# Kernel optimization log

Hardware: AMD Instinct MI355X
Metric: run time of the kernel (lower is better)

Reference implementation:

```python
import jax, jax.numpy as jnp
import numpy as np

B, S, D, H = 2, 2048, 768, 12
HD = D // H


def setup_inputs() -> dict:
    key = jax.random.key(0)
    ks = jax.random.split(key, 8)
    scale = 1.0 / np.sqrt(D)
    inp = {
        "q": jax.random.normal(ks[0], (B, S, D), jnp.float32),
        "k": jax.random.normal(ks[1], (B, S, D), jnp.float32),
        "v": jax.random.normal(ks[2], (B, S, D), jnp.float32),
        # causal mask: 1.0 where attention is disallowed (upper triangle)
        "mask": jnp.triu(jnp.ones((S, S), jnp.float32), k=1)[None, None, :, :],
        "Wq": jax.random.normal(ks[3], (D, D), jnp.float32) * scale,
        "bq": jnp.zeros((D,), jnp.float32),
        "Wk": jax.random.normal(ks[4], (D, D), jnp.float32) * scale,
        "bk": jnp.zeros((D,), jnp.float32),
        "Wv": jax.random.normal(ks[5], (D, D), jnp.float32) * scale,
        "bv": jnp.zeros((D,), jnp.float32),
        "Wo": jax.random.normal(ks[6], (D, D), jnp.float32) * scale,
        "bo": jnp.zeros((D,), jnp.float32),
    }
    return inp


def _split_heads(x):
    # [B, S, D] -> [B, H, S, HD]
    b, s, _ = x.shape
    return x.reshape(b, s, H, HD).transpose(0, 2, 1, 3)


def reference(q, k, v, mask, Wq, bq, Wk, bk, Wv, bv, Wo, bo):
    qh = _split_heads(q @ Wq + bq)
    kh = _split_heads(k @ Wk + bk)
    vh = _split_heads(v @ Wv + bv)
    scale = 1.0 / jnp.sqrt(jnp.asarray(HD, qh.dtype))
    # [B, H, Sq, Sk] — full attention matrix, as in the original
    scores = jnp.einsum("bhqd,bhkd->bhqk", qh, kh) * scale
    scores = scores + mask * -1e9
    attn = jax.nn.softmax(scores, axis=-1)  # dropout is identity at inference
    out = jnp.einsum("bhqk,bhkd->bhqd", attn, vh)
    out = out.transpose(0, 2, 1, 3).reshape(q.shape[0], -1, D)
    return out @ Wo + bo
```

## Files before the change

### kernel.cpp

```cpp
#include <hip/hip_runtime.h>

#define SEQ    2048
#define NB     2
#define DMODEL 768
#define NH     12
#define HDIM   64
#define BS     (NB * SEQ)

typedef __bf16  bf16x8  __attribute__((ext_vector_type(8)));
typedef ushort  ushort8 __attribute__((ext_vector_type(8)));
typedef float   floatx4 __attribute__((ext_vector_type(4)));

#define GLOBAL_AS __attribute__((address_space(1)))
#define LDS_AS    __attribute__((address_space(3)))

union PackU8 { ushort u[8]; uint4 v; };
union PackU4 { ushort u[4]; uint2 v; };

__device__ __forceinline__ ushort f2bf(float x) {
    union { float f; unsigned u; } t; t.f = x;
    unsigned r = t.u + 0x7fffu + ((t.u >> 16) & 1u);
    return (ushort)(r >> 16);
}

__device__ __forceinline__ bf16x8 ld_frag(const ushort* p) {
    return __builtin_bit_cast(bf16x8, *(const ushort8*)p);
}

__global__ void convert_x(const float* __restrict__ q, const float* __restrict__ k,
                          const float* __restrict__ v,
                          ushort* __restrict__ qo, ushort* __restrict__ ko,
                          ushort* __restrict__ vo)
{
    const float* src = blockIdx.z == 0 ? q : blockIdx.z == 1 ? k : v;
    ushort*      dst = blockIdx.z == 0 ? qo : blockIdx.z == 1 ? ko : vo;
    const int i = (blockIdx.x * 256 + threadIdx.x) * 4;
    const float4 f = *(const float4*)(src + i);
    ushort4 o;
    o.x = f2bf(f.x); o.y = f2bf(f.y); o.z = f2bf(f.z); o.w = f2bf(f.w);
    *(ushort4*)(dst + i) = o;
}

__global__ __launch_bounds__(256)
void convert_wT(const float* __restrict__ wq, const float* __restrict__ wk,
                const float* __restrict__ wv, const float* __restrict__ wo,
                ushort* __restrict__ wtcat, ushort* __restrict__ wto)
{
    __shared__ float Tf[64][69];
    const int z = blockIdx.z;
    const float* w = z == 0 ? wq : z == 1 ? wk : z == 2 ? wv : wo;
    ushort*      o = z < 3 ? wtcat + (size_t)z * DMODEL * DMODEL : wto;
    const int k0 = blockIdx.x * 64, n0 = blockIdx.y * 64;
    const int tid = threadIdx.x;
#pragma unroll
    for (int p = 0; p < 4; ++p) {
        const int idx = tid + p * 256;
        const int r = idx >> 4, c = (idx & 15) * 4;
        const float4 f = *(const float4*)&w[(size_t)(k0 + r) * DMODEL + n0 + c];
        Tf[r][c] = f.x; Tf[r][c + 1] = f.y; Tf[r][c + 2] = f.z; Tf[r][c + 3] = f.w;
    }
    __syncthreads();
#pragma unroll
    for (int p = 0; p < 2; ++p) {
        const int idx = tid + p * 256;
        const int n = idx >> 3, kk = (idx & 7) * 8;
        PackU8 pk;
#pragma unroll
        for (int j = 0; j < 8; ++j) pk.u[j] = f2bf(Tf[kk + j][n]);
        *(uint4*)&o[(size_t)(n0 + n) * DMODEL + k0 + kk] = pk.v;
    }
}

__global__ __launch_bounds__(256)
void gemm_qkv(const ushort* __restrict__ xq, const ushort* __restrict__ xk,
              const ushort* __restrict__ xv, const ushort* __restrict__ WT,
              const float* __restrict__ bq, const float* __restrict__ bk,
              const float* __restrict__ bv,
              ushort* __restrict__ oq, ushort* __restrict__ ok,
              ushort* __restrict__ ov)
{
    __shared__ __align__(16) ushort As[128 * 32];
    __shared__ __align__(16) ushort Bs[128 * 32];

    const int z = blockIdx.y / 6;
    const ushort* X = z == 0 ? xq : z == 1 ? xk : xv;

    const int tid  = threadIdx.x;
    const int lane = tid & 63;
    const int w    = tid >> 6;
    const int l15  = lane & 15;
    const int quad = lane >> 4;
    const int wm   = (w >> 1) * 64;
    const int wn   = (w & 1) * 64;
    const int row0 = blockIdx.x * 128;
    const int col0 = blockIdx.y * 128;

    floatx4 acc[4][4];
    const floatx4 fzero = {0.f, 0.f, 0.f, 0.f};
#pragma unroll
    for (int i = 0; i < 4; ++i)
#pragma unroll
        for (int j = 0; j < 4; ++j) acc[i][j] = fzero;

    const int rin = lane >> 2;
    const int gc  = (lane & 3) * 8;

    for (int k0 = 0; k0 < DMODEL; k0 += 32) {
#pragma unroll
        for (int p = 0; p < 2; ++p) {
            const int ch = w * 2 + p;
            const int r  = ch * 16 + rin;
            __builtin_amdgcn_global_load_lds(
                (const GLOBAL_AS uint*)&X[(size_t)(row0 + r) * DMODEL + k0 + gc],
                (LDS_AS uint*)&As[ch * 512], 16, 0, 0);
            __builtin_amdgcn_global_load_lds(
                (const GLOBAL_AS uint*)&WT[(size_t)(col0 + r) * DMODEL + k0 + gc],
                (LDS_AS uint*)&Bs[ch * 512], 16, 0, 0);
        }
        __syncthreads();

        bf16x8 af[4], bfr[4];
#pragma unroll
        for (int t = 0; t < 4; ++t) {
            af[t]  = ld_frag(&As[(wm + t * 16 + l15) * 32 + quad * 8]);
            bfr[t] = ld_frag(&Bs[(wn + t * 16 + l15) * 32 + quad * 8]);
        }
#pragma unroll
        for (int ti = 0; ti < 4; ++ti)
#pragma unroll
            for (int tj = 0; tj < 4; ++tj)
                acc[ti][tj] = __builtin_amdgcn_mfma_f32_16x16x32_bf16(
                    af[ti], bfr[tj], acc[ti][tj], 0, 0, 0);
        __syncthreads();
    }

    const int c0 = (blockIdx.y % 6) * 128;
    const float*  bias = z == 0 ? bq : z == 1 ? bk : bv;
    ushort*       out  = z == 0 ? oq : z == 1 ? ok : ov;
    const float   sc   = (z == 0) ? 0.18033688f : 1.f;
#pragma unroll
    for (int tj = 0; tj < 4; ++tj) {
        const int c_l = c0 + wn + tj * 16 + l15;
        const float bb = bias[c_l];
        const int h  = c_l >> 6;
        const int dd = c_l & 63;
#pragma unroll
        for (int ti = 0; ti < 4; ++ti) {
#pragma unroll
            for (int ri = 0; ri < 4; ++ri) {
                const int r_g = row0 + wm + ti * 16 + quad * 4 + ri;
                const int b   = r_g >> 11;
                const int s   = r_g & (SEQ - 1);
                out[(((size_t)(b * NH + h) * SEQ + s) << 6) + dd] =
                    f2bf((acc[ti][tj][ri] + bb) * sc);
            }
        }
    }
}

__global__ __launch_bounds__(256)
void gemm_out(const ushort* __restrict__ X, const ushort* __restrict__ WT,
              const float* __restrict__ bias, float* __restrict__ fo)
{
    __shared__ __align__(16) ushort As[64][40];
    __shared__ __align__(16) ushort Bs[128][40];

    const int tid  = threadIdx.x;
    const int lane = tid & 63;
    const int wv   = tid >> 6;
    const int wm   = (wv >> 1) * 32;
    const int wn   = (wv & 1) * 64;
    const int l15  = lane & 15;
    const int quad = lane >> 4;
    const int row0 = blockIdx.x * 64;
    const int col0 = blockIdx.y * 128;

    floatx4 acc[2][4];
    const floatx4 fzero = {0.f, 0.f, 0.f, 0.f};
#pragma unroll
    for (int i = 0; i < 2; ++i)
#pragma unroll
        for (int j = 0; j < 4; ++j) acc[i][j] = fzero;

    const int sr = tid >> 2;
    const int sc = (tid & 3) * 8;

    for (int k0 = 0; k0 < DMODEL; k0 += 32) {
        *(uint4*)&As[sr][sc] = *(const uint4*)&X[(size_t)(row0 + sr) * DMODEL + k0 + sc];
#pragma unroll
        for (int p = 0; p < 2; ++p) {
            const int r = sr + p * 64;
            *(uint4*)&Bs[r][sc] = *(const uint4*)&WT[(size_t)(col0 + r) * DMODEL + k0 + sc];
        }
        __syncthreads();

        bf16x8 af[2], bfr[4];
#pragma unroll
        for (int t = 0; t < 2; ++t)
            af[t] = ld_frag(&As[wm + t * 16 + l15][quad * 8]);
#pragma unroll
        for (int t = 0; t < 4; ++t)
            bfr[t] = ld_frag(&Bs[wn + t * 16 + l15][quad * 8]);
#pragma unroll
        for (int ti = 0; ti < 2; ++ti)
#pragma unroll
            for (int tj = 0; tj < 4; ++tj)
                acc[ti][tj] = __builtin_amdgcn_mfma_f32_16x16x32_bf16(
                    af[ti], bfr[tj], acc[ti][tj], 0, 0, 0);
        __syncthreads();
    }

#pragma unroll
    for (int tj = 0; tj < 4; ++tj) {
        const int c_g = col0 + wn + tj * 16 + l15;
        const float bb = bias[c_g];
#pragma unroll
        for (int ti = 0; ti < 2; ++ti)
#pragma unroll
            for (int ri = 0; ri < 4; ++ri) {
                const int r_g = row0 + wm + ti * 16 + quad * 4 + ri;
                fo[(size_t)r_g * DMODEL + c_g] = acc[ti][tj][ri] + bb;
            }
    }
}

__global__ void transpose_v(const ushort* __restrict__ vh, ushort* __restrict__ vt)
{
    __shared__ __align__(16) ushort T[64][72];
    const int bh = blockIdx.y;
    const int s0 = blockIdx.x * 64;
    const ushort* src = vh + (size_t)bh * SEQ * HDIM;
    ushort*       dst = vt + (size_t)bh * HDIM * SEQ;

#pragma unroll
    for (int p = 0; p < 2; ++p) {
        const int idx = threadIdx.x + p * 256;
        const int r = idx >> 3, c = (idx & 7) * 8;
        *(uint4*)&T[r][c] = *(const uint4*)&src[(size_t)(s0 + r) * HDIM + c];
    }
    __syncthreads();
#pragma unroll
    for (int p = 0; p < 2; ++p) {
        const int idx = threadIdx.x + p * 256;
        const int d = idx >> 3, c = (idx & 7) * 8;
        PackU8 pk;
#pragma unroll
        for (int j = 0; j < 8; ++j) pk.u[j] = T[c + j][d];
        *(uint4*)&dst[(size_t)d * SEQ + s0 + c] = pk.v;
    }
}

__global__ __launch_bounds__(64)
void attn_mfma(const ushort* __restrict__ qh, const ushort* __restrict__ kh,
               const ushort* __restrict__ vt, ushort* __restrict__ ctx)
{
    __shared__ __align__(16) ushort Ks[2][64][64];
    __shared__ __align__(16) ushort Vs[2][64][64];
    __shared__ __align__(16) ushort Ps[32][64];

    const int lane = threadIdx.x;
    const int l15  = lane & 15;
    const int quad = lane >> 4;
    const int e3   = l15 & 7;

    const int id  = blockIdx.x;
    const int xcd = id & 7;
    const int jj  = id >> 3;
    const int g   = jj >> 5;
    const int x   = jj & 31;
    const int bh  = xcd + 8 * g;
    const int b   = bh / NH, h = bh - b * NH;
    const int qA  = x, qB = 63 - x;
    const int nkA = (qA >> 1) + 1;
    const size_t base = (size_t)bh * SEQ * HDIM;

    bf16x8 qA0[2], qA1[2], qB0[2], qB1[2];
#pragma unroll
    for (int ks = 0; ks < 2; ++ks) {
        qA0[ks] = ld_frag(&qh[base + (size_t)(qA * 32 +      l15) * HDIM + ks * 32 + quad * 8]);
        qA1[ks] = ld_frag(&qh[base + (size_t)(qA * 32 + 16 + l15) * HDIM + ks * 32 + quad * 8]);
        qB0[ks] = ld_frag(&qh[base + (size_t)(qB * 32 +      l15) * HDIM + ks * 32 + quad * 8]);
        qB1[ks] = ld_frag(&qh[base + (size_t)(qB * 32 + 16 + l15) * HDIM + ks * 32 + quad * 8]);
    }

    const int sr8  = lane >> 3;
    const int kcol = ((lane & 7) ^ sr8) * 8;

    auto stage = [&](int bufi, int c0s) {
#pragma unroll
        for (int p = 0; p < 8; ++p) {
            __builtin_amdgcn_global_load_lds(
                (const GLOBAL_AS uint*)&kh[base + (size_t)(c0s + 8 * p + sr8) * HDIM + kcol],
                (LDS_AS uint*)&Ks[bufi][8 * p][0], 16, 0, 0);
            __builtin_amdgcn_global_load_lds(
                (const GLOBAL_AS uint*)&vt[base + (size_t)(8 * p + sr8) * SEQ + c0s + kcol],
                (LDS_AS uint*)&Vs[bufi][8 * p][0], 16, 0, 0);
        }
    };

    stage(0, 0);

    float l0 = 0.f, l1 = 0.f;
    floatx4 O[4][2];
    const floatx4 fzero = {0.f, 0.f, 0.f, 0.f};
#pragma unroll
    for (int dj = 0; dj < 4; ++dj) { O[dj][0] = fzero; O[dj][1] = fzero; }

    auto epilogue = [&](int qt) {
        const float i0 = 1.f / l0, i1 = 1.f / l1;
        float ib0[4], ib1[4];
#pragma unroll
        for (int ri = 0; ri < 4; ++ri) {
            ib0[ri] = __shfl(i0, quad * 4 + ri);
            ib1[ri] = __shfl(i1, quad * 4 + ri);
        }
#pragma unroll
        for (int dj = 0; dj < 4; ++dj)
#pragma unroll
            for (int ri = 0; ri < 4; ++ri) {
                const int r0 = qt * 32 + quad * 4 + ri;
                ctx[((size_t)b * SEQ + r0) * DMODEL + h * HDIM + dj * 16 + l15] =
                    f2bf(O[dj][0][ri] * ib0[ri]);
                ctx[((size_t)b * SEQ + r0 + 16) * DMODEL + h * HDIM + dj * 16 + l15] =
                    f2bf(O[dj][1][ri] * ib1[ri]);
            }
    };

    asm volatile("s_waitcnt vmcnt(0)" ::: "memory");

    for (int t = 0; t <= 32; ++t) {
        const int  cur  = t & 1;
        const bool isA  = (t < nkA);
        const int  kt   = isA ? t : t - nkA;
        const int  c0   = kt * 64;
        const bool diag = (t == nkA - 1) || (t == 32);
        const int  qt   = isA ? qA : qB;

        bf16x8 kf[4][2], vf[4][2];
#pragma unroll
        for (int nj = 0; nj < 4; ++nj)
#pragma unroll
            for (int ks = 0; ks < 2; ++ks) {
                kf[nj][ks] = ld_frag(&Ks[cur][nj * 16 + l15][(ks * 32 + quad * 8) ^ (e3 << 3)]);
                vf[nj][ks] = ld_frag(&Vs[cur][nj * 16 + l15][(ks * 32 + quad * 8) ^ (e3 << 3)]);
            }

        if (t < 32) {
            const int kn = (t + 1 < nkA) ? (t + 1) : (t + 1 - nkA);
            stage(cur ^ 1, kn * 64);
        }

        const bf16x8 q0k0 = isA ? qA0[0] : qB0[0];
        const bf16x8 q0k1 = isA ? qA0[1] : qB0[1];
        const bf16x8 q1k0 = isA ? qA1[0] : qB1[0];
        const bf16x8 q1k1 = isA ? qA1[1] : qB1[1];

        floatx4 S[4][2];
        __builtin_amdgcn_s_setprio(1);
#pragma unroll
        for (int nj = 0; nj < 4; ++nj) {
            S[nj][0] = __builtin_amdgcn_mfma_f32_16x16x32_bf16(kf[nj][0], q0k0, fzero, 0, 0, 0);
            S[nj][1] = __builtin_amdgcn_mfma_f32_16x16x32_bf16(kf[nj][0], q1k0, fzero, 0, 0, 0);
            S[nj][0] = __builtin_amdgcn_mfma_f32_16x16x32_bf16(kf[nj][1], q0k1, S[nj][0], 0, 0, 0);
            S[nj][1] = __builtin_amdgcn_mfma_f32_16x16x32_bf16(kf[nj][1], q1k1, S[nj][1], 0, 0, 0);
        }
        __builtin_amdgcn_s_setprio(0);

        float rs0 = 0.f, rs1 = 0.f;
        const int rg0 = qt * 32 + l15;
#pragma unroll
        for (int nj = 0; nj < 4; ++nj) {
            PackU4 p0, p1;
#pragma unroll
            for (int ri = 0; ri < 4; ++ri) {
                const int krow = c0 + nj * 16 + quad * 4 + ri;
                float v0 = __builtin_amdgcn_exp2f(S[nj][0][ri]);
                float v1 = __builtin_amdgcn_exp2f(S[nj][1][ri]);
                if (diag) {
                    if (krow > rg0)      v0 = 0.f;
                    if (krow > rg0 + 16) v1 = 0.f;
                }
                rs0 += v0; rs1 += v1;
                union { float f; unsigned u; } t0, t1;
                t0.f = v0; t1.f = v1;
                p0.u[ri] = (ushort)(t0.u >> 16);
                p1.u[ri] = (ushort)(t1.u >> 16);
            }
            *(uint2*)&Ps[l15     ][(nj * 16 + quad * 4) ^ (e3 << 3)] = p0.v;
            *(uint2*)&Ps[16 + l15][(nj * 16 + quad * 4) ^ (e3 << 3)] = p1.v;
        }
        rs0 += __shfl_xor(rs0, 16); rs0 += __shfl_xor(rs0, 32);
        rs1 += __shfl_xor(rs1, 16); rs1 += __shfl_xor(rs1, 32);
        l0 += rs0; l1 += rs1;

        bf16x8 pf0[2], pf1[2];
#pragma unroll
        for (int ks = 0; ks < 2; ++ks) {
            pf0[ks] = ld_frag(&Ps[l15     ][(ks * 32 + quad * 8) ^ (e3 << 3)]);
            pf1[ks] = ld_frag(&Ps[16 + l15][(ks * 32 + quad * 8) ^ (e3 << 3)]);
        }

        __builtin_amdgcn_s_setprio(1);
#pragma unroll
        for (int dj = 0; dj < 4; ++dj)
#pragma unroll
            for (int ks = 0; ks < 2; ++ks) {
                O[dj][0] = __builtin_amdgcn_mfma_f32_16x16x32_bf16(pf0[ks], vf[dj][ks], O[dj][0], 0, 0, 0);
                O[dj][1] = __builtin_amdgcn_mfma_f32_16x16x32_bf16(pf1[ks], vf[dj][ks], O[dj][1], 0, 0, 0);
            }
        __builtin_amdgcn_s_setprio(0);

        if (t == nkA - 1) {
            epilogue(qA);
            l0 = 0.f; l1 = 0.f;
#pragma unroll
            for (int dj = 0; dj < 4; ++dj) { O[dj][0] = fzero; O[dj][1] = fzero; }
        }

        asm volatile("s_waitcnt vmcnt(0)" ::: "memory");
    }

    epilogue(qB);
}

extern "C" void kernel_launch(void* const* d_in, const int* in_sizes, int n_in,
                              void* d_out, int out_size, void* d_ws, size_t ws_size,
                              hipStream_t stream)
{
    const float* q  = (const float*)d_in[0];
    const float* k  = (const float*)d_in[1];
    const float* v  = (const float*)d_in[2];
    const float* Wq = (const float*)d_in[4];
    const float* bq = (const float*)d_in[5];
    const float* Wk = (const float*)d_in[6];
    const float* bk = (const float*)d_in[7];
    const float* Wv = (const float*)d_in[8];
    const float* bv = (const float*)d_in[9];
    const float* Wo = (const float*)d_in[10];
    const float* bo = (const float*)d_in[11];
    float* out = (float*)d_out;

    char* ws = (char*)d_ws;
    const size_t ACT = (size_t)BS * DMODEL * 2;
    ushort* qx    = (ushort*)(ws);
    ushort* kx    = (ushort*)(ws + ACT);
    ushort* vx    = (ushort*)(ws + 2 * ACT);
    ushort* qhp   = (ushort*)(ws + 3 * ACT);
    ushort* khp   = (ushort*)(ws + 4 * ACT);
    ushort* vhp   = (ushort*)(ws + 5 * ACT);
    ushort* wtcat = (ushort*)(ws + 6 * ACT);
    ushort* wto   = wtcat + (size_t)3 * DMODEL * DMODEL;
    ushort* vhT   = vx;
    ushort* ctx   = qx;

    convert_x<<<dim3(BS * DMODEL / 1024, 1, 3), 256, 0, stream>>>(q, k, v, qx, kx, vx);
    convert_wT<<<dim3(12, 12, 4), 256, 0, stream>>>(Wq, Wk, Wv, Wo, wtcat, wto);
    gemm_qkv<<<dim3(BS / 128, 18), 256, 0, stream>>>(
        qx, kx, vx, wtcat, bq, bk, bv, qhp, khp, vhp);
    transpose_v<<<dim3(SEQ / 64, NB * NH), 256, 0, stream>>>(vhp, vhT);
    attn_mfma<<<dim3(768), 64, 0, stream>>>(qhp, khp, vhT, ctx);
    gemm_out<<<dim3(BS / 64, DMODEL / 128), 256, 0, stream>>>(ctx, wto, bo, out);
}
```

Measured before the change: 210.9 us.

## Load K/V fragments directly from global, one q-tile per block, doubled grid

The attention kernel no longer pairs two query tiles per block or stages K/V tiles into LDS with global_load_lds double buffering. Each block now handles a single 32-row query tile, with the heaviest tiles scheduled first, and reads K and V^T MFMA fragments straight from global memory into registers. K fragments are ping-ponged across two register sets to overlap loads with compute, and the grid doubles to 1536 blocks. This removes LDS traffic and loop-carried pair bookkeeping, at the cost of uncoalesced global fragment reads, higher register pressure and less balanced per-block work.

```diff
diff --git a/kernel.cpp b/kernel.cpp
--- a/kernel.cpp
+++ b/kernel.cpp
@@ -254,8 +254,6 @@
 void attn_mfma(const ushort* __restrict__ qh, const ushort* __restrict__ kh,
                const ushort* __restrict__ vt, ushort* __restrict__ ctx)
 {
-    __shared__ __align__(16) ushort Ks[2][64][64];
-    __shared__ __align__(16) ushort Vs[2][64][64];
     __shared__ __align__(16) ushort Ps[32][64];
 
     const int lane = threadIdx.x;
@@ -266,39 +264,19 @@
     const int id  = blockIdx.x;
     const int xcd = id & 7;
     const int jj  = id >> 3;
-    const int g   = jj >> 5;
-    const int x   = jj & 31;
+    const int g   = jj >> 6;
+    const int qt  = 63 - (jj & 63);
     const int bh  = xcd + 8 * g;
     const int b   = bh / NH, h = bh - b * NH;
-    const int qA  = x, qB = 63 - x;
-    const int nkA = (qA >> 1) + 1;
+    const int nk  = (qt >> 1) + 1;
     const size_t base = (size_t)bh * SEQ * HDIM;
 
-    bf16x8 qA0[2], qA1[2], qB0[2], qB1[2];
+    bf16x8 qf0[2], qf1[2];
 #pragma unroll
     for (int ks = 0; ks < 2; ++ks) {
-        qA0[ks] = ld_frag(&qh[base + (size_t)(qA * 32 +      l15) * HDIM + ks * 32 + quad * 8]);
-        qA1[ks] = ld_frag(&qh[base + (size_t)(qA * 32 + 16 + l15) * HDIM + ks * 32 + quad * 8]);
-        qB0[ks] = ld_frag(&qh[base + (size_t)(qB * 32 +      l15) * HDIM + ks * 32 + quad * 8]);
-        qB1[ks] = ld_frag(&qh[base + (size_t)(qB * 32 + 16 + l15) * HDIM + ks * 32 + quad * 8]);
-    }
-
-    const int sr8  = lane >> 3;
-    const int kcol = ((lane & 7) ^ sr8) * 8;
-
-    auto stage = [&](int bufi, int c0s) {
-#pragma unroll
-        for (int p = 0; p < 8; ++p) {
-            __builtin_amdgcn_global_load_lds(
-                (const GLOBAL_AS uint*)&kh[base + (size_t)(c0s + 8 * p + sr8) * HDIM + kcol],
-                (LDS_AS uint*)&Ks[bufi][8 * p][0], 16, 0, 0);
-            __builtin_amdgcn_global_load_lds(
-                (const GLOBAL_AS uint*)&vt[base + (size_t)(8 * p + sr8) * SEQ + c0s + kcol],
-                (LDS_AS uint*)&Vs[bufi][8 * p][0], 16, 0, 0);
-        }
-    };
-
-    stage(0, 0);
+        qf0[ks] = ld_frag(&qh[base + (size_t)(qt * 32 +      l15) * HDIM + ks * 32 + quad * 8]);
+        qf1[ks] = ld_frag(&qh[base + (size_t)(qt * 32 + 16 + l15) * HDIM + ks * 32 + quad * 8]);
+    }
 
     float l0 = 0.f, l1 = 0.f;
     floatx4 O[4][2];
@@ -306,68 +284,42 @@
 #pragma unroll
     for (int dj = 0; dj < 4; ++dj) { O[dj][0] = fzero; O[dj][1] = fzero; }
 
-    auto epilogue = [&](int qt) {
-        const float i0 = 1.f / l0, i1 = 1.f / l1;
-        float ib0[4], ib1[4];
-#pragma unroll
-        for (int ri = 0; ri < 4; ++ri) {
-            ib0[ri] = __shfl(i0, quad * 4 + ri);
-            ib1[ri] = __shfl(i1, quad * 4 + ri);
-        }
+    const int rg0 = qt * 32 + l15;
+
+    auto load_k = [&](bf16x8 (&kf)[4][2], int t) {
+        const int c0 = t * 64;
+#pragma unroll
+        for (int nj = 0; nj < 4; ++nj)
+#pragma unroll
+            for (int ks = 0; ks < 2; ++ks)
+                kf[nj][ks] = ld_frag(
+                    &kh[base + (size_t)(c0 + nj * 16 + l15) * HDIM + ks * 32 + quad * 8]);
+    };
+
+    auto body = [&](const bf16x8 (&kf)[4][2], int t) {
+        const int  c0   = t * 64;
+        const bool diag = (t == nk - 1);
+
+        bf16x8 vf[4][2];
 #pragma unroll
         for (int dj = 0; dj < 4; ++dj)
 #pragma unroll
-            for (int ri = 0; ri < 4; ++ri) {
-                const int r0 = qt * 32 + quad * 4 + ri;
-                ctx[((size_t)b * SEQ + r0) * DMODEL + h * HDIM + dj * 16 + l15] =
-                    f2bf(O[dj][0][ri] * ib0[ri]);
-                ctx[((size_t)b * SEQ + r0 + 16) * DMODEL + h * HDIM + dj * 16 + l15] =
-                    f2bf(O[dj][1][ri] * ib1[ri]);
-            }
-    };
-
-    asm volatile("s_waitcnt vmcnt(0)" ::: "memory");
-
-    for (int t = 0; t <= 32; ++t) {
-        const int  cur  = t & 1;
-        const bool isA  = (t < nkA);
-        const int  kt   = isA ? t : t - nkA;
-        const int  c0   = kt * 64;
-        const bool diag = (t == nkA - 1) || (t == 32);
-        const int  qt   = isA ? qA : qB;
-
-        bf16x8 kf[4][2], vf[4][2];
-#pragma unroll
-        for (int nj = 0; nj < 4; ++nj)
-#pragma unroll
-            for (int ks = 0; ks < 2; ++ks) {
-                kf[nj][ks] = ld_frag(&Ks[cur][nj * 16 + l15][(ks * 32 + quad * 8) ^ (e3 << 3)]);
-                vf[nj][ks] = ld_frag(&Vs[cur][nj * 16 + l15][(ks * 32 + quad * 8) ^ (e3 << 3)]);
-            }
-
-        if (t < 32) {
-            const int kn = (t + 1 < nkA) ? (t + 1) : (t + 1 - nkA);
-            stage(cur ^ 1, kn * 64);
-        }
-
-        const bf16x8 q0k0 = isA ? qA0[0] : qB0[0];
-        const bf16x8 q0k1 = isA ? qA0[1] : qB0[1];
-        const bf16x8 q1k0 = isA ? qA1[0] : qB1[0];
-        const bf16x8 q1k1 = isA ? qA1[1] : qB1[1];
+            for (int ks = 0; ks < 2; ++ks)
+                vf[dj][ks] = ld_frag(
+                    &vt[base + (size_t)(dj * 16 + l15) * SEQ + c0 + ks * 32 + quad * 8]);
 
         floatx4 S[4][2];
         __builtin_amdgcn_s_setprio(1);
 #pragma unroll
         for (int nj = 0; nj < 4; ++nj) {
-            S[nj][0] = __builtin_amdgcn_mfma_f32_16x16x32_bf16(kf[nj][0], q0k0, fzero, 0, 0, 0);
-            S[nj][1] = __builtin_amdgcn_mfma_f32_16x16x32_bf16(kf[nj][0], q1k0, fzero, 0, 0, 0);
-            S[nj][0] = __builtin_amdgcn_mfma_f32_16x16x32_bf16(kf[nj][1], q0k1, S[nj][0], 0, 0, 0);
-            S[nj][1] = __builtin_amdgcn_mfma_f32_16x16x32_bf16(kf[nj][1], q1k1, S[nj][1], 0, 0, 0);
+            S[nj][0] = __builtin_amdgcn_mfma_f32_16x16x32_bf16(kf[nj][0], qf0[0], fzero, 0, 0, 0);
+            S[nj][1] = __builtin_amdgcn_mfma_f32_16x16x32_bf16(kf[nj][0], qf1[0], fzero, 0, 0, 0);
+            S[nj][0] = __builtin_amdgcn_mfma_f32_16x16x32_bf16(kf[nj][1], qf0[1], S[nj][0], 0, 0, 0);
+            S[nj][1] = __builtin_amdgcn_mfma_f32_16x16x32_bf16(kf[nj][1], qf1[1], S[nj][1], 0, 0, 0);
         }
         __builtin_amdgcn_s_setprio(0);
 
         float rs0 = 0.f, rs1 = 0.f;
-        const int rg0 = qt * 32 + l15;
 #pragma unroll
         for (int nj = 0; nj < 4; ++nj) {
             PackU4 p0, p1;
@@ -409,18 +361,36 @@
                 O[dj][1] = __builtin_amdgcn_mfma_f32_16x16x32_bf16(pf1[ks], vf[dj][ks], O[dj][1], 0, 0, 0);
             }
         __builtin_amdgcn_s_setprio(0);
-
-        if (t == nkA - 1) {
-            epilogue(qA);
-            l0 = 0.f; l1 = 0.f;
-#pragma unroll
-            for (int dj = 0; dj < 4; ++dj) { O[dj][0] = fzero; O[dj][1] = fzero; }
-        }
-
-        asm volatile("s_waitcnt vmcnt(0)" ::: "memory");
-    }
-
-    epilogue(qB);
+    };
+
+    bf16x8 kfA[4][2], kfB[4][2];
+    load_k(kfA, 0);
+    int t = 0;
+    for (; t + 1 < nk; t += 2) {
+        load_k(kfB, t + 1);
+        body(kfA, t);
+        if (t + 2 < nk) load_k(kfA, t + 2);
+        body(kfB, t + 1);
+    }
+    if (t < nk) body(kfA, t);
+
+    const float i0 = 1.f / l0, i1 = 1.f / l1;
+    float ib0[4], ib1[4];
+#pragma unroll
+    for (int ri = 0; ri < 4; ++ri) {
+        ib0[ri] = __shfl(i0, quad * 4 + ri);
+        ib1[ri] = __shfl(i1, quad * 4 + ri);
+    }
+#pragma unroll
+    for (int dj = 0; dj < 4; ++dj)
+#pragma unroll
+        for (int ri = 0; ri < 4; ++ri) {
+            const int r0 = qt * 32 + quad * 4 + ri;
+            ctx[((size_t)b * SEQ + r0) * DMODEL + h * HDIM + dj * 16 + l15] =
+                f2bf(O[dj][0][ri] * ib0[ri]);
+            ctx[((size_t)b * SEQ + r0 + 16) * DMODEL + h * HDIM + dj * 16 + l15] =
+                f2bf(O[dj][1][ri] * ib1[ri]);
+        }
 }
 
 extern "C" void kernel_launch(void* const* d_in, const int* in_sizes, int n_in,
@@ -458,6 +428,6 @@
     gemm_qkv<<<dim3(BS / 128, 18), 256, 0, stream>>>(
         qx, kx, vx, wtcat, bq, bk, bv, qhp, khp, vhp);
     transpose_v<<<dim3(SEQ / 64, NB * NH), 256, 0, stream>>>(vhp, vhT);
-    attn_mfma<<<dim3(768), 64, 0, stream>>>(qhp, khp, vhT, ctx);
+    attn_mfma<<<dim3(1536), 64, 0, stream>>>(qhp, khp, vhT, ctx);
     gemm_out<<<dim3(BS / 64, DMODEL / 128), 256, 0, stream>>>(ctx, wto, bo, out);
 }
```

Result: no change. 213.2 us (+1.1%).
